# Performance work log

Measured on AMD Instinct MI355X. Metric: run time of the kernel, lower is better.

## Reference

```python
import jax, jax.numpy as jnp
import numpy as np

T = 512          # tokens
H = 2048         # hidden_size
E = 256          # n_routed_experts (8 groups x 32)
G = 8            # tucker groups
EPG = 32         # experts per group
K = 6            # top_k
I = 1408         # moe_intermediate_size
R1 = 128         # tucker input rank
R2 = 128         # tucker output rank


def setup_inputs() -> dict:
    key = jax.random.key(0)
    ks = jax.random.split(key, 12)
    s = 0.02
    return {
        "hidden_states": jax.random.normal(ks[0], (T, H), jnp.float32),
        "w_router": jax.random.normal(ks[1], (H, E), jnp.float32) * s,
        # gate_proj Tucker factors: H -> I
        "U_in_gate": jax.random.normal(ks[2], (G, H, R1), jnp.float32) * s,
        "core_gate": jax.random.normal(ks[3], (E, R1, R2), jnp.float32) * s,
        "U_out_gate": jax.random.normal(ks[4], (G, I, R2), jnp.float32) * s,
        # up_proj Tucker factors: H -> I
        "U_in_up": jax.random.normal(ks[5], (G, H, R1), jnp.float32) * s,
        "core_up": jax.random.normal(ks[6], (E, R1, R2), jnp.float32) * s,
        "U_out_up": jax.random.normal(ks[7], (G, I, R2), jnp.float32) * s,
        # down_proj Tucker factors: I -> H
        "U_in_down": jax.random.normal(ks[8], (G, I, R1), jnp.float32) * s,
        "core_down": jax.random.normal(ks[9], (E, R1, R2), jnp.float32) * s,
        "U_out_down": jax.random.normal(ks[10], (G, H, R2), jnp.float32) * s,
    }


def _tucker_apply(x, g, e, U_in, core, U_out):
    """Per-expert Tucker linear: y_t = ((x_t @ U_in[g_t]) @ core[e_t]) @ U_out[g_t].T
    x: [Td, din]; g: [Td] group ids; e: [Td] full expert ids.
    U_in: [G, din, r1]; core: [E, r1, r2]; U_out: [G, dout, r2]."""
    h1 = jnp.einsum('td,gdr->tgr', x, U_in)                       # [Td, G, r1]
    h1 = jnp.take_along_axis(h1, g[:, None, None], axis=1)[:, 0]  # [Td, r1]
    h2 = jnp.einsum('tr,trs->ts', h1, core[e])                    # [Td, r2]
    y = jnp.einsum('ts,gds->tgd', h2, U_out)                      # [Td, G, dout]
    return jnp.take_along_axis(y, g[:, None, None], axis=1)[:, 0]


def reference(hidden_states, w_router, U_in_gate, core_gate, U_out_gate,
              U_in_up, core_up, U_out_up, U_in_down, core_down, U_out_down):
    n_tok, hid = hidden_states.shape
    router_logits = hidden_states @ w_router                          # [T, E]
    probs = jax.nn.softmax(router_logits.astype(jnp.float32), axis=-1)
    routing_weights, selected = jax.lax.top_k(probs, K)               # [T, K]
    routing_weights = routing_weights / routing_weights.sum(-1, keepdims=True)
    routing_weights = routing_weights.astype(hidden_states.dtype)

    xd = jnp.repeat(hidden_states, K, axis=0)                         # [T*K, H]
    e = selected.reshape(-1)                                          # [T*K]
    g = e // EPG                                                      # group ids

    gate_out = _tucker_apply(xd, g, e, U_in_gate, core_gate, U_out_gate)
    up_out = _tucker_apply(xd, g, e, U_in_up, core_up, U_out_up)
    inter = jax.nn.silu(gate_out) * up_out                            # [T*K, I]
    down_out = _tucker_apply(inter, g, e, U_in_down, core_down, U_out_down)

    combined = (down_out.reshape(n_tok, K, hid) * routing_weights[..., None]).sum(axis=1)
    return combined
```

## Files before the change

### kernel.cpp

```cpp
#include <hip/hip_runtime.h>
#include <cmath>
#include <cstdint>

#define TNUM 512
#define HID 2048
#define NEXP 256
#define NGRP 8
#define KTOP 6
#define IDIM 1408
#define RNK 128
#define NPAIR (TNUM*KTOP)
#define NRCAP 3328
#define MAXTILES (NRCAP/32)

typedef _Float16 f16;
typedef f16  f16x8 __attribute__((ext_vector_type(8)));
typedef f16  f16x4 __attribute__((ext_vector_type(4)));
typedef float f32x4 __attribute__((ext_vector_type(4)));
#define MFMA16(a,b,c) __builtin_amdgcn_mfma_f32_16x16x32_f16((a),(b),(c),0,0,0)

static __device__ __forceinline__ float4 ld4(const float* p){ return *reinterpret_cast<const float4*>(p); }
static __device__ __forceinline__ void st4(float* p, float4 v){ *reinterpret_cast<float4*>(p) = v; }
static __device__ __forceinline__ f16x8 ldh8(const f16* p){ return *reinterpret_cast<const f16x8*>(p); }

constexpr size_t A256(size_t x){ return (x + 255) & ~(size_t)255; }
constexpr size_t OFF_SEL    = 0;
constexpr size_t OFF_WT     = A256(OFF_SEL    + (size_t)NPAIR*4);
constexpr size_t OFF_CNT    = A256(OFF_WT     + (size_t)NPAIR*4);
constexpr size_t OFF_ESTART = A256(OFF_CNT    + (size_t)NEXP*4);
constexpr size_t OFF_TG     = A256(OFF_ESTART + (size_t)NEXP*4);
constexpr size_t OFF_HDR    = A256(OFF_TG     + (size_t)MAXTILES*4);
constexpr size_t OFF_ROWT   = A256(OFF_HDR    + 16);
constexpr size_t OFF_POS    = A256(OFF_ROWT   + (size_t)NRCAP*4);
constexpr size_t OFF_BIG    = A256(OFF_POS    + (size_t)NPAIR*4);

constexpr size_t SZ_XH    = (size_t)TNUM*HID*2;
constexpr size_t SZ_UTI   = (size_t)NGRP*RNK*HID*2;
constexpr size_t SZ_H1ALL = (size_t)2*TNUM*NGRP*RNK*2;
constexpr size_t SZ_UO    = (size_t)NGRP*IDIM*RNK*2;
constexpr size_t SZ_UOD   = (size_t)NGRP*HID*RNK*2;
constexpr size_t SZ_WR    = (size_t)NEXP*HID*2;
constexpr size_t SZ_H2    = (size_t)NRCAP*RNK*2;
constexpr size_t SZ_DOWNO = (size_t)NRCAP*HID*2;

constexpr size_t OFF_XH    = OFF_BIG;
constexpr size_t OFF_XL    = OFF_XH   + SZ_XH;
constexpr size_t OFF_UTIG  = OFF_XL   + SZ_XH;
constexpr size_t OFF_UTIU  = OFF_UTIG + SZ_UTI;
constexpr size_t OFF_H1    = OFF_UTIU + SZ_UTI;
constexpr size_t REG_END   = OFF_H1   + SZ_H1ALL;
constexpr size_t OFF_DOWNO = OFF_XH;
constexpr size_t OFF_LPART = OFF_H1;
constexpr size_t OFF_UOG   = REG_END;
constexpr size_t OFF_UOU   = OFF_UOG  + SZ_UO;
constexpr size_t OFF_UTID  = OFF_UOU  + SZ_UO;
constexpr size_t OFF_UOD   = OFF_UTID + SZ_UO;
constexpr size_t OFF_WRH   = OFF_UOD  + SZ_UOD;
constexpr size_t OFF_WRL   = OFF_WRH  + SZ_WR;
constexpr size_t OFF_H2G   = OFF_WRL  + SZ_WR;
constexpr size_t OFF_H2U   = OFF_H2G  + SZ_H2;
constexpr size_t OFF_D1P   = OFF_H2U  + SZ_H2;
constexpr size_t OFF_D2    = OFF_D1P  + 4*SZ_H2;
constexpr size_t WS_NEED   = OFF_D2   + SZ_H2;
static_assert(OFF_DOWNO + SZ_DOWNO <= OFF_UOG, "downo overlay must end before persistent tail");

__global__ __launch_bounds__(256) void k_cvt(
    const float* __restrict__ x,   const float* __restrict__ Uog,
    const float* __restrict__ Uou, const float* __restrict__ Uod,
    const float* __restrict__ wr,
    const float* __restrict__ Uig, const float* __restrict__ Uiu, const float* __restrict__ Uid,
    f16* __restrict__ xh, f16* __restrict__ xl,
    f16* __restrict__ uog, f16* __restrict__ uou, f16* __restrict__ uod,
    f16* __restrict__ wh, f16* __restrict__ wl,
    f16* __restrict__ ig, f16* __restrict__ iu, f16* __restrict__ idn,
    int* __restrict__ cnt){
  __shared__ float tile[32][33];
  const int b = blockIdx.x, tid = threadIdx.x;
  if(b < 1024){
    const size_t i = (size_t)b*256 + tid;
    float4 v = ld4(x + i*4);
    f16x4 H, L;
    H[0]=(f16)v.x; L[0]=(f16)(v.x-(float)H[0]);
    H[1]=(f16)v.y; L[1]=(f16)(v.y-(float)H[1]);
    H[2]=(f16)v.z; L[2]=(f16)(v.z-(float)H[2]);
    H[3]=(f16)v.w; L[3]=(f16)(v.w-(float)H[3]);
    *reinterpret_cast<f16x4*>(xh + i*4) = H;
    *reinterpret_cast<f16x4*>(xl + i*4) = L;
    return;
  }
  if(b < 5888){
    const float* in; f16* hi; size_t i;
    if(b < 2432){        in = Uog; hi = uog; i = (size_t)(b-1024)*256 + tid; }
    else if(b < 3840){   in = Uou; hi = uou; i = (size_t)(b-2432)*256 + tid; }
    else {               in = Uod; hi = uod; i = (size_t)(b-3840)*256 + tid; }
    float4 v = ld4(in + i*4);
    f16x4 H;
    H[0]=(f16)(v.x*16.f); H[1]=(f16)(v.y*16.f); H[2]=(f16)(v.z*16.f); H[3]=(f16)(v.w*16.f);
    *reinterpret_cast<f16x4*>(hi + i*4) = H;
    return;
  }
  if(b < 6400){
    const int wb = b - 5888;
    if(wb == 0) cnt[tid] = 0;
    const int c0 = (wb & 7)*32, r0 = (wb >> 3)*32;
    { const int r = tid>>3, c4 = (tid&7)*4;
      float4 v = ld4(wr + (size_t)(r0+r)*NEXP + c0 + c4);
      tile[r][c4]=v.x; tile[r][c4+1]=v.y; tile[r][c4+2]=v.z; tile[r][c4+3]=v.w; }
    __syncthreads();
    { const int c = tid>>3, r4 = (tid&7)*4;
      f16x4 H, L;
      #pragma unroll
      for(int k = 0; k < 4; k++){
        float v = tile[r4+k][c]*16.f;
        H[k] = (f16)v; L[k] = (f16)(v - (float)H[k]);
      }
      const size_t o = (size_t)(c0+c)*HID + r0 + r4;
      *reinterpret_cast<f16x4*>(wh + o) = H;
      *reinterpret_cast<f16x4*>(wl + o) = L; }
    return;
  }
  const int b2 = b - 6400;
  const int cx = b2 & 3, ry = (b2>>2) & 63, z = b2 >> 8;
  const int tensor = z >> 3, g = z & 7;
  const float* in; f16* o; int R;
  if(tensor == 0){ in = Uig; o = ig; R = HID; }
  else if(tensor == 1){ in = Uiu; o = iu; R = HID; }
  else { in = Uid; o = idn; R = IDIM; }
  const int r0 = ry*32, c0 = cx*32;
  if(r0 >= R) return;
  in += (size_t)g*R*RNK; o += (size_t)g*RNK*R;
  { const int r = tid>>3, c4 = (tid&7)*4;
    float4 v = ld4(in + (size_t)(r0+r)*RNK + c0 + c4);
    tile[r][c4]=v.x; tile[r][c4+1]=v.y; tile[r][c4+2]=v.z; tile[r][c4+3]=v.w; }
  __syncthreads();
  { const int c = tid>>3, r4 = (tid&7)*4;
    f16x4 H;
    #pragma unroll
    for(int k = 0; k < 4; k++) H[k] = (f16)(tile[r4+k][c]*16.f);
    *reinterpret_cast<f16x4*>(o + (size_t)(c0+c)*R + r0 + r4) = H; }
}

__global__ __launch_bounds__(256) void k_router_mfma(
    const f16* __restrict__ xh, const f16* __restrict__ xl,
    const f16* __restrict__ wh, const f16* __restrict__ wl,
    float* __restrict__ lpart){
  __shared__ float red[4][32][64];
  const int m = blockIdx.x, ecol = blockIdx.y, kz = blockIdx.z;
  const int tid = threadIdx.x;
  const int wid = tid>>6, lane = tid&63, q = lane>>4, id = lane&15;
  const int r0 = m*32, e0 = ecol*64;
  const int kb = kz*512 + wid*128;
  f32x4 acc[2][4];
  #pragma unroll
  for(int f = 0; f < 2; f++)
    #pragma unroll
    for(int c = 0; c < 4; c++) acc[f][c] = (f32x4){0.f,0.f,0.f,0.f};
  #pragma unroll
  for(int kk = 0; kk < 128; kk += 32){
    const size_t a0 = (size_t)(r0+id)*HID    + kb + kk + q*8;
    const size_t a1 = (size_t)(r0+16+id)*HID + kb + kk + q*8;
    f16x8 ah0 = ldh8(xh + a0), al0 = ldh8(xl + a0);
    f16x8 ah1 = ldh8(xh + a1), al1 = ldh8(xl + a1);
    #pragma unroll
    for(int c = 0; c < 4; c++){
      const size_t bo = (size_t)(e0 + c*16 + id)*HID + kb + kk + q*8;
      f16x8 bh = ldh8(wh + bo);
      f16x8 bl = ldh8(wl + bo);
      acc[0][c] = MFMA16(ah0, bh, acc[0][c]);
      acc[0][c] = MFMA16(ah0, bl, acc[0][c]);
      acc[0][c] = MFMA16(al0, bh, acc[0][c]);
      acc[1][c] = MFMA16(ah1, bh, acc[1][c]);
      acc[1][c] = MFMA16(ah1, bl, acc[1][c]);
      acc[1][c] = MFMA16(al1, bh, acc[1][c]);
    }
  }
  #pragma unroll
  for(int f = 0; f < 2; f++)
    #pragma unroll
    for(int c = 0; c < 4; c++)
      #pragma unroll
      for(int r = 0; r < 4; r++)
        red[wid][f*16 + q*4 + r][c*16 + id] = acc[f][c][r];
  __syncthreads();
  const int row = tid>>3, c8 = (tid&7)*8;
  float o[8];
  #pragma unroll
  for(int j = 0; j < 8; j++)
    o[j] = (red[0][row][c8+j] + red[1][row][c8+j] + red[2][row][c8+j] + red[3][row][c8+j])*0.0625f;
  float* dst = &lpart[((size_t)kz*TNUM + r0 + row)*NEXP + e0 + c8];
  st4(dst,     make_float4(o[0],o[1],o[2],o[3]));
  st4(dst + 4, make_float4(o[4],o[5],o[6],o[7]));
}

__global__ __launch_bounds__(256) void k_topk(const float* __restrict__ lpart,
                                              int* __restrict__ sel,
                                              float* __restrict__ wt,
                                              int* __restrict__ cnt){
  __shared__ float wv[4];
  __shared__ int   wi[4];
  __shared__ float swin[KTOP];
  __shared__ int   iwin[KTOP];
  const int t = blockIdx.x, tid = threadIdx.x;
  const int lane = tid & 63, wid = tid >> 6;
  const size_t base = (size_t)t*NEXP + tid;
  float v = lpart[base] + lpart[base + (size_t)TNUM*NEXP]
          + lpart[base + (size_t)2*TNUM*NEXP] + lpart[base + (size_t)3*TNUM*NEXP];
  for(int k = 0; k < KTOP; k++){
    float cv = v; int ci = tid;
    #pragma unroll
    for(int off = 1; off < 64; off <<= 1){
      float ov = __shfl_xor(cv, off);
      int   oi = __shfl_xor(ci, off);
      if(ov > cv || (ov == cv && oi < ci)){ cv = ov; ci = oi; }
    }
    if(lane == 0){ wv[wid] = cv; wi[wid] = ci; }
    __syncthreads();
    if(tid == 0){
      float bv = wv[0]; int bi = wi[0];
      #pragma unroll
      for(int w2 = 1; w2 < 4; w2++)
        if(wv[w2] > bv || (wv[w2] == bv && wi[w2] < bi)){ bv = wv[w2]; bi = wi[w2]; }
      swin[k] = bv; iwin[k] = bi;
    }
    __syncthreads();
    if(tid == iwin[k]) v = -INFINITY;
  }
  if(tid == 0){
    float mx = swin[0], s = 0.f, ww[KTOP];
    #pragma unroll
    for(int k = 0; k < KTOP; k++){ ww[k] = expf(swin[k]-mx); s += ww[k]; }
    float inv = 1.f/s;
    #pragma unroll
    for(int k = 0; k < KTOP; k++){
      sel[t*KTOP+k] = iwin[k];
      wt[t*KTOP+k]  = ww[k]*inv;
      atomicAdd(&cnt[iwin[k]], 1);
    }
  }
}

__global__ __launch_bounds__(256) void k_meta_scatter(
    const int* __restrict__ cnt, const int* __restrict__ sel,
    int* __restrict__ estart, int* __restrict__ tile_group, int* __restrict__ hdr,
    int* __restrict__ row_t, int* __restrict__ pos_of_pair){
  __shared__ int scnt[256];
  __shared__ int gsum[8];
  __shared__ int g0[9];
  __shared__ int curs[256];
  const int tid = threadIdx.x;
  scnt[tid] = cnt[tid];
  if(tid < 8) gsum[tid] = 0;
  __syncthreads();
  atomicAdd(&gsum[tid>>5], scnt[tid]);
  __syncthreads();
  if(tid == 0){
    int run = 0;
    for(int g = 0; g < 8; g++){ g0[g] = run; run += (gsum[g]+31) & ~31; }
    g0[8] = run; hdr[0] = run>>5; hdr[1] = run;
  }
  __syncthreads();
  int g = tid >> 5, s = g0[g];
  for(int i = (g<<5); i < tid; i++) s += scnt[i];
  estart[tid] = s; curs[tid] = s;
  const int nt = g0[8] >> 5;
  for(int t2 = tid; t2 < MAXTILES; t2 += 256){
    int gg = -1;
    if(t2 < nt){
      for(int g2 = 0; g2 < 8; g2++) if(t2*32 >= g0[g2] && t2*32 < g0[g2+1]) gg = g2;
    }
    tile_group[t2] = gg;
  }
  __syncthreads();
  for(int p = tid; p < NPAIR; p += 256){
    const int e = sel[p];
    const int pos = atomicAdd(&curs[e], 1);
    row_t[pos] = p / KTOP;
    pos_of_pair[p] = pos;
  }
}

__global__ __launch_bounds__(256) void k_mm_stage1(
    const f16* __restrict__ xh,
    const f16* __restrict__ Bg_, const f16* __restrict__ Bu_,
    f16* __restrict__ H1){
  __shared__ float red[4][32][64];
  const int nt = blockIdx.x, m = blockIdx.y;
  const int pu = nt>>4, g = (nt>>1)&7, ch = nt&1;
  const f16* B = (pu ? Bu_ : Bg_) + (size_t)g*RNK*HID + (size_t)ch*64*HID;
  const int tid = threadIdx.x;
  const int wid = tid>>6, lane = tid&63, q = lane>>4, id = lane&15;
  const int kb = wid*512;
  const int r0 = m*32;
  f32x4 acc[2][4];
  #pragma unroll
  for(int f = 0; f < 2; f++)
    #pragma unroll
    for(int c = 0; c < 4; c++) acc[f][c] = (f32x4){0.f,0.f,0.f,0.f};
  #pragma unroll 4
  for(int kk = 0; kk < 512; kk += 32){
    f16x8 a0 = ldh8(xh + (size_t)(r0+id)*HID    + kb + kk + q*8);
    f16x8 a1 = ldh8(xh + (size_t)(r0+16+id)*HID + kb + kk + q*8);
    #pragma unroll
    for(int c = 0; c < 4; c++){
      f16x8 b = ldh8(B + (size_t)(c*16+id)*HID + kb + kk + q*8);
      acc[0][c] = MFMA16(a0, b, acc[0][c]);
      acc[1][c] = MFMA16(a1, b, acc[1][c]);
    }
  }
  #pragma unroll
  for(int f = 0; f < 2; f++)
    #pragma unroll
    for(int c = 0; c < 4; c++)
      #pragma unroll
      for(int r = 0; r < 4; r++)
        red[wid][f*16 + q*4 + r][c*16 + id] = acc[f][c][r];
  __syncthreads();
  f16* out = H1 + (size_t)pu*TNUM*(NGRP*RNK);
  const int row = tid>>3, c8 = (tid&7)*8;
  f16x8 o8;
  #pragma unroll
  for(int j = 0; j < 8; j++)
    o8[j] = (f16)(red[0][row][c8+j] + red[1][row][c8+j] + red[2][row][c8+j] + red[3][row][c8+j]);
  *reinterpret_cast<f16x8*>(&out[(size_t)(r0+row)*(NGRP*RNK) + g*RNK + ch*64 + c8]) = o8;
}

__global__ __launch_bounds__(256) void k_core2(
    const float* __restrict__ Cg, const float* __restrict__ Cu,
    const f16* __restrict__ H1,
    const int* __restrict__ estart, const int* __restrict__ cnt,
    const int* __restrict__ row_t,
    f16* __restrict__ h2g, f16* __restrict__ h2u){
  __shared__ f16 Cs[RNK][RNK+8];
  __shared__ float tile[32][33];
  const int e = blockIdx.x, up = blockIdx.y;
  const int n = cnt[e];
  if(n == 0) return;
  const float* Cf = (up ? Cu : Cg) + (size_t)e*RNK*RNK;
  const int tid = threadIdx.x;
  #pragma unroll 2
  for(int st = 0; st < 16; st++){
    const int R0 = (st>>2)*32, C0 = (st&3)*32;
    { const int r = tid>>3, c4 = (tid&7)*4;
      float4 v = ld4(Cf + (size_t)(R0+r)*RNK + C0 + c4);
      tile[r][c4]=v.x; tile[r][c4+1]=v.y; tile[r][c4+2]=v.z; tile[r][c4+3]=v.w; }
    __syncthreads();
    { const int c = tid>>3, r4 = (tid&7)*4;
      f16x4 H;
      #pragma unroll
      for(int k2 = 0; k2 < 4; k2++) H[k2] = (f16)(tile[r4+k2][c]*16.f);
      *reinterpret_cast<f16x4*>(&Cs[C0+c][R0+r4]) = H; }
    __syncthreads();
  }
  const int j0 = estart[e], g = e >> 5;
  const f16* A = H1 + (size_t)up*TNUM*(NGRP*RNK);
  f16* o = up ? h2u : h2g;
  const int wid = tid>>6, lane = tid&63, q = lane>>4, id = lane&15;
  for(int rt = 0; rt*16 < n; rt++){
    const int jrow = j0 + rt*16 + id;
    const int jj = jrow < j0+n ? jrow : j0;
    const f16* arow = A + (size_t)row_t[jj]*(NGRP*RNK) + g*RNK;
    f32x4 acc0 = (f32x4){0.f,0.f,0.f,0.f};
    f32x4 acc1 = (f32x4){0.f,0.f,0.f,0.f};
    #pragma unroll
    for(int kk = 0; kk < RNK; kk += 32){
      f16x8 a = ldh8(arow + kk + q*8);
      f16x8 b0 = *reinterpret_cast<const f16x8*>(&Cs[wid*32 + id][kk + q*8]);
      f16x8 b1 = *reinterpret_cast<const f16x8*>(&Cs[wid*32 + 16 + id][kk + q*8]);
      acc0 = MFMA16(a, b0, acc0);
      acc1 = MFMA16(a, b1, acc1);
    }
    #pragma unroll
    for(int r = 0; r < 4; r++){
      const int j = j0 + rt*16 + q*4 + r;
      if(j < j0+n){
        o[(size_t)j*RNK + wid*32 + id]      = (f16)acc0[r];
        o[(size_t)j*RNK + wid*32 + 16 + id] = (f16)acc1[r];
      }
    }
  }
}

__global__ __launch_bounds__(256) void k_gateup_downin(
    const f16* __restrict__ Ag, const f16* __restrict__ Au,
    const f16* __restrict__ Bg, const f16* __restrict__ Bu,
    const f16* __restrict__ Bd,
    const int* __restrict__ tg,
    f16* __restrict__ d1p){
  __shared__ f16 inter_s[32][360];
  const int g = tg[blockIdx.x];
  if(g < 0) return;
  const int j0 = blockIdx.x*32, qz = blockIdx.y;
  const int cbase = qz*352;
  const int tid = threadIdx.x, wid = tid>>6, lane = tid&63, q = lane>>4, id = lane&15;
  const size_t bbase = (size_t)g*IDIM*RNK;
  f16x8 aG[2][4], aU[2][4];
  #pragma unroll
  for(int f = 0; f < 2; f++)
    #pragma unroll
    for(int k4 = 0; k4 < 4; k4++){
      const size_t off = (size_t)(j0 + f*16 + id)*RNK + k4*32 + q*8;
      aG[f][k4] = ldh8(Ag + off);
      aU[f][k4] = ldh8(Au + off);
    }
  for(int t = wid; t < 22; t += 4){
    const int c0 = cbase + t*16;
    f32x4 accg0 = (f32x4){0.f,0.f,0.f,0.f}, accg1 = (f32x4){0.f,0.f,0.f,0.f};
    f32x4 accu0 = (f32x4){0.f,0.f,0.f,0.f}, accu1 = (f32x4){0.f,0.f,0.f,0.f};
    #pragma unroll
    for(int k4 = 0; k4 < 4; k4++){
      const size_t bo = bbase + (size_t)(c0 + id)*RNK + k4*32 + q*8;
      f16x8 bg = ldh8(Bg + bo);
      f16x8 bu = ldh8(Bu + bo);
      accg0 = MFMA16(aG[0][k4], bg, accg0);
      accg1 = MFMA16(aG[1][k4], bg, accg1);
      accu0 = MFMA16(aU[0][k4], bu, accu0);
      accu1 = MFMA16(aU[1][k4], bu, accu1);
    }
    #pragma unroll
    for(int r = 0; r < 4; r++){
      float vg0 = accg0[r]*(1.f/4096.f), vu0 = accu0[r]*(1.f/4096.f);
      float vg1 = accg1[r]*(1.f/4096.f), vu1 = accu1[r]*(1.f/4096.f);
      inter_s[q*4+r][t*16+id]    = (f16)(vg0/(1.f+expf(-vg0))*vu0*256.f);
      inter_s[16+q*4+r][t*16+id] = (f16)(vg1/(1.f+expf(-vg1))*vu1*256.f);
    }
  }
  __syncthreads();
  const int col0 = wid*32;
  f32x4 acc[2][2];
  #pragma unroll
  for(int f = 0; f < 2; f++)
    #pragma unroll
    for(int c = 0; c < 2; c++) acc[f][c] = (f32x4){0.f,0.f,0.f,0.f};
  const f16* Bdg = Bd + (size_t)g*RNK*IDIM;
  #pragma unroll 2
  for(int kk = 0; kk < 352; kk += 32){
    f16x8 a0 = *reinterpret_cast<const f16x8*>(&inter_s[id][kk + q*8]);
    f16x8 a1 = *reinterpret_cast<const f16x8*>(&inter_s[16+id][kk + q*8]);
    #pragma unroll
    for(int c = 0; c < 2; c++){
      f16x8 b = ldh8(Bdg + (size_t)(col0 + c*16 + id)*IDIM + cbase + kk + q*8);
      acc[0][c] = MFMA16(a0, b, acc[0][c]);
      acc[1][c] = MFMA16(a1, b, acc[1][c]);
    }
  }
  f16* out = d1p + (size_t)qz*NRCAP*RNK;
  #pragma unroll
  for(int f = 0; f < 2; f++)
    #pragma unroll
    for(int c = 0; c < 2; c++)
      #pragma unroll
      for(int r = 0; r < 4; r++)
        out[(size_t)(j0 + f*16 + q*4 + r)*RNK + col0 + c*16 + id] = (f16)acc[f][c][r];
}

__global__ __launch_bounds__(256) void k_core_down(
    const float* __restrict__ Cd,
    const f16* __restrict__ d1p,
    const int* __restrict__ estart, const int* __restrict__ cnt,
    f16* __restrict__ d2){
  __shared__ f16 Cs[RNK][RNK+8];
  __shared__ float tile[32][33];
  const int e = blockIdx.x;
  const int n = cnt[e];
  if(n == 0) return;
  const float* Cf = Cd + (size_t)e*RNK*RNK;
  const int tid = threadIdx.x;
  #pragma unroll 2
  for(int st = 0; st < 16; st++){
    const int R0 = (st>>2)*32, C0 = (st&3)*32;
    { const int r = tid>>3, c4 = (tid&7)*4;
      float4 v = ld4(Cf + (size_t)(R0+r)*RNK + C0 + c4);
      tile[r][c4]=v.x; tile[r][c4+1]=v.y; tile[r][c4+2]=v.z; tile[r][c4+3]=v.w; }
    __syncthreads();
    { const int c = tid>>3, r4 = (tid&7)*4;
      f16x4 H;
      #pragma unroll
      for(int k2 = 0; k2 < 4; k2++) H[k2] = (f16)(tile[r4+k2][c]*16.f);
      *reinterpret_cast<f16x4*>(&Cs[C0+c][R0+r4]) = H; }
    __syncthreads();
  }
  const int j0 = estart[e];
  const size_t PL = (size_t)NRCAP*RNK;
  const int wid = tid>>6, lane = tid&63, q = lane>>4, id = lane&15;
  for(int rt = 0; rt*16 < n; rt++){
    const int jrow = j0 + rt*16 + id;
    const int jj = jrow < j0+n ? jrow : j0;
    const size_t arow = (size_t)jj*RNK;
    f32x4 acc0 = (f32x4){0.f,0.f,0.f,0.f};
    f32x4 acc1 = (f32x4){0.f,0.f,0.f,0.f};
    #pragma unroll
    for(int kk = 0; kk < RNK; kk += 32){
      const size_t off = arow + kk + q*8;
      f16x8 a = ldh8(d1p + off);
      a += ldh8(d1p + off + PL);
      a += ldh8(d1p + off + 2*PL);
      a += ldh8(d1p + off + 3*PL);
      f16x8 b0 = *reinterpret_cast<const f16x8*>(&Cs[wid*32 + id][kk + q*8]);
      f16x8 b1 = *reinterpret_cast<const f16x8*>(&Cs[wid*32 + 16 + id][kk + q*8]);
      acc0 = MFMA16(a, b0, acc0);
      acc1 = MFMA16(a, b1, acc1);
    }
    #pragma unroll
    for(int r = 0; r < 4; r++){
      const int j = j0 + rt*16 + q*4 + r;
      if(j < j0+n){
        d2[(size_t)j*RNK + wid*32 + id]      = (f16)acc0[r];
        d2[(size_t)j*RNK + wid*32 + 16 + id] = (f16)acc1[r];
      }
    }
  }
}

__global__ __launch_bounds__(128) void k_mm_down_out(
    const f16* __restrict__ A_, const f16* __restrict__ B_,
    const int* __restrict__ tg,
    f16* __restrict__ downo){
  const int g = tg[blockIdx.x];
  if(g < 0) return;
  const int j0 = blockIdx.x*32;
  const f16* B = B_ + (size_t)g*HID*RNK;
  const int tid = threadIdx.x;
  const int wid = tid>>6, lane = tid&63, q = lane>>4, id = lane&15;
  const int c0 = blockIdx.y*128 + wid*64;
  f32x4 acc[2][4];
  #pragma unroll
  for(int f = 0; f < 2; f++)
    #pragma unroll
    for(int c = 0; c < 4; c++) acc[f][c] = (f32x4){0.f,0.f,0.f,0.f};
  #pragma unroll 2
  for(int kk = 0; kk < RNK; kk += 32){
    f16x8 a0 = ldh8(A_ + (size_t)(j0+id)*RNK    + kk + q*8);
    f16x8 a1 = ldh8(A_ + (size_t)(j0+16+id)*RNK + kk + q*8);
    #pragma unroll
    for(int c = 0; c < 4; c++){
      f16x8 b = ldh8(B + (size_t)(c0 + c*16 + id)*RNK + kk + q*8);
      acc[0][c] = MFMA16(a0, b, acc[0][c]);
      acc[1][c] = MFMA16(a1, b, acc[1][c]);
    }
  }
  #pragma unroll
  for(int f = 0; f < 2; f++)
    #pragma unroll
    for(int c = 0; c < 4; c++)
      #pragma unroll
      for(int r = 0; r < 4; r++)
        downo[(size_t)(j0 + f*16 + q*4 + r)*HID + c0 + c*16 + id] = (f16)(acc[f][c][r]*(1.f/1024.f));
}

__global__ __launch_bounds__(256) void k_combine(const f16* __restrict__ downo,
                                                 const int* __restrict__ pos_of_pair,
                                                 const float* __restrict__ wt,
                                                 float* __restrict__ out){
  const int idx = blockIdx.x*256 + threadIdx.x;
  const int t  = idx >> 9;
  const int h4 = (idx & 511) << 2;
  float4 acc = make_float4(0.f,0.f,0.f,0.f);
  #pragma unroll
  for(int k = 0; k < KTOP; k++){
    const int p = t*KTOP + k;
    const float w = wt[p]*(1.f/1024.f);
    const int pos = pos_of_pair[p];
    f16x4 v = *reinterpret_cast<const f16x4*>(&downo[(size_t)pos*HID + h4]);
    acc.x += w*(float)v[0]; acc.y += w*(float)v[1];
    acc.z += w*(float)v[2]; acc.w += w*(float)v[3];
  }
  st4(&out[(size_t)t*HID + h4], acc);
}

extern "C" void kernel_launch(void* const* d_in, const int* in_sizes, int n_in,
                              void* d_out, int out_size, void* d_ws, size_t ws_size,
                              hipStream_t stream){
  const float* x   = (const float*)d_in[0];
  const float* wr  = (const float*)d_in[1];
  const float* Uig = (const float*)d_in[2];
  const float* cg  = (const float*)d_in[3];
  const float* Uog = (const float*)d_in[4];
  const float* Uiu = (const float*)d_in[5];
  const float* cu  = (const float*)d_in[6];
  const float* Uou = (const float*)d_in[7];
  const float* Uid = (const float*)d_in[8];
  const float* cd  = (const float*)d_in[9];
  const float* Uod = (const float*)d_in[10];
  float* out = (float*)d_out;
  char* ws = (char*)d_ws;
  if(ws_size < WS_NEED) return;

  int*   sel    = (int*)  (ws + OFF_SEL);
  float* wt     = (float*)(ws + OFF_WT);
  int*   cnt    = (int*)  (ws + OFF_CNT);
  int*   estart = (int*)  (ws + OFF_ESTART);
  int*   tg     = (int*)  (ws + OFF_TG);
  int*   hdr    = (int*)  (ws + OFF_HDR);
  int*   row_t  = (int*)  (ws + OFF_ROWT);
  int*   pos    = (int*)  (ws + OFF_POS);
  float* lpart  = (float*)(ws + OFF_LPART);
  f16* xh    = (f16*)(ws + OFF_XH);
  f16* xl    = (f16*)(ws + OFF_XL);
  f16* utig  = (f16*)(ws + OFF_UTIG);
  f16* utiu  = (f16*)(ws + OFF_UTIU);
  f16* H1    = (f16*)(ws + OFF_H1);
  f16* uog   = (f16*)(ws + OFF_UOG);
  f16* uou   = (f16*)(ws + OFF_UOU);
  f16* utid  = (f16*)(ws + OFF_UTID);
  f16* uod   = (f16*)(ws + OFF_UOD);
  f16* wrh   = (f16*)(ws + OFF_WRH);
  f16* wrl   = (f16*)(ws + OFF_WRL);
  f16* h2g   = (f16*)(ws + OFF_H2G);
  f16* h2u   = (f16*)(ws + OFF_H2U);
  f16* d1p   = (f16*)(ws + OFF_D1P);
  f16* d2    = (f16*)(ws + OFF_D2);
  f16* downo = (f16*)(ws + OFF_DOWNO);

  k_cvt      <<<12544,             256, 0, stream>>>(x, Uog, Uou, Uod, wr, Uig, Uiu, Uid,
                                                     xh, xl, uog, uou, uod, wrh, wrl,
                                                     utig, utiu, utid, cnt);

  k_router_mfma<<<dim3(16,4,4),    256, 0, stream>>>(xh, xl, wrh, wrl, lpart);
  k_topk     <<<TNUM,              256, 0, stream>>>(lpart, sel, wt, cnt);
  k_meta_scatter<<<1,              256, 0, stream>>>(cnt, sel, estart, tg, hdr, row_t, pos);

  k_mm_stage1<<<dim3(32,16),       256, 0, stream>>>(xh, utig, utiu, H1);
  k_core2    <<<dim3(NEXP,2),      256, 0, stream>>>(cg, cu, H1, estart, cnt, row_t, h2g, h2u);
  k_gateup_downin<<<dim3(MAXTILES,4),256,0, stream>>>(h2g, h2u, uog, uou, utid, tg, d1p);
  k_core_down<<<NEXP,              256, 0, stream>>>(cd, d1p, estart, cnt, d2);
  k_mm_down_out<<<dim3(MAXTILES,16),128,0, stream>>>(d2, uod, tg, downo);
  k_combine  <<<1024,              256, 0, stream>>>(downo, pos, wt, out);
}
```

Before: 136.7 us.

## Fuse top-k and routing metadata via last-block counter; narrow stage1 tiles

The separate single-block metadata scatter kernel is folded into the top-k kernel. Each block increments a global done counter after a threadfence, and the last block to finish builds the expert offsets, tile groups and row mappings. This removes one kernel launch and its gap. Separately, stage-1 projection tiles shrink from 64 to 32 output columns, doubling the grid to 1024 blocks for better occupancy, at the cost of reloading the activation rows twice as often.

Result: slower. 150.1 us (+9.9%).

```diff
diff --git a/kernel.cpp b/kernel.cpp
--- a/kernel.cpp
+++ b/kernel.cpp
@@ -30,7 +30,8 @@
 constexpr size_t OFF_ESTART = A256(OFF_CNT    + (size_t)NEXP*4);
 constexpr size_t OFF_TG     = A256(OFF_ESTART + (size_t)NEXP*4);
 constexpr size_t OFF_HDR    = A256(OFF_TG     + (size_t)MAXTILES*4);
-constexpr size_t OFF_ROWT   = A256(OFF_HDR    + 16);
+constexpr size_t OFF_DONE   = A256(OFF_HDR    + 16);
+constexpr size_t OFF_ROWT   = A256(OFF_DONE   + 16);
 constexpr size_t OFF_POS    = A256(OFF_ROWT   + (size_t)NRCAP*4);
 constexpr size_t OFF_BIG    = A256(OFF_POS    + (size_t)NPAIR*4);
 
@@ -73,7 +74,7 @@
     f16* __restrict__ uog, f16* __restrict__ uou, f16* __restrict__ uod,
     f16* __restrict__ wh, f16* __restrict__ wl,
     f16* __restrict__ ig, f16* __restrict__ iu, f16* __restrict__ idn,
-    int* __restrict__ cnt){
+    int* __restrict__ cnt, int* __restrict__ done){
   __shared__ float tile[32][33];
   const int b = blockIdx.x, tid = threadIdx.x;
   if(b < 1024){
@@ -101,7 +102,7 @@
   }
   if(b < 6400){
     const int wb = b - 5888;
-    if(wb == 0) cnt[tid] = 0;
+    if(wb == 0){ cnt[tid] = 0; if(tid == 0) done[0] = 0; }
     const int c0 = (wb & 7)*32, r0 = (wb >> 3)*32;
     { const int r = tid>>3, c4 = (tid&7)*4;
       float4 v = ld4(wr + (size_t)(r0+r)*NEXP + c0 + c4);
@@ -192,14 +193,21 @@
   st4(dst + 4, make_float4(o[4],o[5],o[6],o[7]));
 }
 
-__global__ __launch_bounds__(256) void k_topk(const float* __restrict__ lpart,
-                                              int* __restrict__ sel,
-                                              float* __restrict__ wt,
-                                              int* __restrict__ cnt){
+__global__ __launch_bounds__(256) void k_topk_meta(
+    const float* __restrict__ lpart,
+    int* __restrict__ sel, float* __restrict__ wt, int* __restrict__ cnt,
+    int* __restrict__ done,
+    int* __restrict__ estart, int* __restrict__ tile_group, int* __restrict__ hdr,
+    int* __restrict__ row_t, int* __restrict__ pos_of_pair){
   __shared__ float wv[4];
   __shared__ int   wi[4];
   __shared__ float swin[KTOP];
   __shared__ int   iwin[KTOP];
+  __shared__ int   lastflag;
+  __shared__ int scnt[256];
+  __shared__ int gsum[8];
+  __shared__ int g0[9];
+  __shared__ int curs[256];
   const int t = blockIdx.x, tid = threadIdx.x;
   const int lane = tid & 63, wid = tid >> 6;
   const size_t base = (size_t)t*NEXP + tid;
@@ -236,18 +244,13 @@
       wt[t*KTOP+k]  = ww[k]*inv;
       atomicAdd(&cnt[iwin[k]], 1);
     }
-  }
-}
-
-__global__ __launch_bounds__(256) void k_meta_scatter(
-    const int* __restrict__ cnt, const int* __restrict__ sel,
-    int* __restrict__ estart, int* __restrict__ tile_group, int* __restrict__ hdr,
-    int* __restrict__ row_t, int* __restrict__ pos_of_pair){
-  __shared__ int scnt[256];
-  __shared__ int gsum[8];
-  __shared__ int g0[9];
-  __shared__ int curs[256];
-  const int tid = threadIdx.x;
+    __threadfence();
+    const int old = atomicAdd(done, 1);
+    lastflag = (old == TNUM-1) ? 1 : 0;
+  }
+  __syncthreads();
+  if(!lastflag) return;
+  __threadfence();
   scnt[tid] = cnt[tid];
   if(tid < 8) gsum[tid] = 0;
   __syncthreads();
@@ -283,25 +286,25 @@
     const f16* __restrict__ xh,
     const f16* __restrict__ Bg_, const f16* __restrict__ Bu_,
     f16* __restrict__ H1){
-  __shared__ float red[4][32][64];
+  __shared__ float red[4][32][32];
   const int nt = blockIdx.x, m = blockIdx.y;
-  const int pu = nt>>4, g = (nt>>1)&7, ch = nt&1;
-  const f16* B = (pu ? Bu_ : Bg_) + (size_t)g*RNK*HID + (size_t)ch*64*HID;
+  const int pu = nt>>5, g = (nt>>2)&7, ch = nt&3;
+  const f16* B = (pu ? Bu_ : Bg_) + (size_t)g*RNK*HID + (size_t)ch*32*HID;
   const int tid = threadIdx.x;
   const int wid = tid>>6, lane = tid&63, q = lane>>4, id = lane&15;
   const int kb = wid*512;
   const int r0 = m*32;
-  f32x4 acc[2][4];
-  #pragma unroll
-  for(int f = 0; f < 2; f++)
-    #pragma unroll
-    for(int c = 0; c < 4; c++) acc[f][c] = (f32x4){0.f,0.f,0.f,0.f};
+  f32x4 acc[2][2];
+  #pragma unroll
+  for(int f = 0; f < 2; f++)
+    #pragma unroll
+    for(int c = 0; c < 2; c++) acc[f][c] = (f32x4){0.f,0.f,0.f,0.f};
   #pragma unroll 4
   for(int kk = 0; kk < 512; kk += 32){
     f16x8 a0 = ldh8(xh + (size_t)(r0+id)*HID    + kb + kk + q*8);
     f16x8 a1 = ldh8(xh + (size_t)(r0+16+id)*HID + kb + kk + q*8);
     #pragma unroll
-    for(int c = 0; c < 4; c++){
+    for(int c = 0; c < 2; c++){
       f16x8 b = ldh8(B + (size_t)(c*16+id)*HID + kb + kk + q*8);
       acc[0][c] = MFMA16(a0, b, acc[0][c]);
       acc[1][c] = MFMA16(a1, b, acc[1][c]);
@@ -310,18 +313,18 @@
   #pragma unroll
   for(int f = 0; f < 2; f++)
     #pragma unroll
-    for(int c = 0; c < 4; c++)
+    for(int c = 0; c < 2; c++)
       #pragma unroll
       for(int r = 0; r < 4; r++)
         red[wid][f*16 + q*4 + r][c*16 + id] = acc[f][c][r];
   __syncthreads();
   f16* out = H1 + (size_t)pu*TNUM*(NGRP*RNK);
-  const int row = tid>>3, c8 = (tid&7)*8;
-  f16x8 o8;
-  #pragma unroll
-  for(int j = 0; j < 8; j++)
-    o8[j] = (f16)(red[0][row][c8+j] + red[1][row][c8+j] + red[2][row][c8+j] + red[3][row][c8+j]);
-  *reinterpret_cast<f16x8*>(&out[(size_t)(r0+row)*(NGRP*RNK) + g*RNK + ch*64 + c8]) = o8;
+  const int row = tid>>3, c4 = (tid&7)*4;
+  f16x4 o4;
+  #pragma unroll
+  for(int j = 0; j < 4; j++)
+    o4[j] = (f16)(red[0][row][c4+j] + red[1][row][c4+j] + red[2][row][c4+j] + red[3][row][c4+j]);
+  *reinterpret_cast<f16x4*>(&out[(size_t)(r0+row)*(NGRP*RNK) + g*RNK + ch*32 + c4]) = o4;
 }
 
 __global__ __launch_bounds__(256) void k_core2(
@@ -591,6 +594,7 @@
   int*   estart = (int*)  (ws + OFF_ESTART);
   int*   tg     = (int*)  (ws + OFF_TG);
   int*   hdr    = (int*)  (ws + OFF_HDR);
+  int*   done   = (int*)  (ws + OFF_DONE);
   int*   row_t  = (int*)  (ws + OFF_ROWT);
   int*   pos    = (int*)  (ws + OFF_POS);
   float* lpart  = (float*)(ws + OFF_LPART);
@@ -613,13 +617,13 @@
 
   k_cvt      <<<12544,             256, 0, stream>>>(x, Uog, Uou, Uod, wr, Uig, Uiu, Uid,
                                                      xh, xl, uog, uou, uod, wrh, wrl,
-                                                     utig, utiu, utid, cnt);
+                                                     utig, utiu, utid, cnt, done);
 
   k_router_mfma<<<dim3(16,4,4),    256, 0, stream>>>(xh, xl, wrh, wrl, lpart);
-  k_topk     <<<TNUM,              256, 0, stream>>>(lpart, sel, wt, cnt);
-  k_meta_scatter<<<1,              256, 0, stream>>>(cnt, sel, estart, tg, hdr, row_t, pos);
-
-  k_mm_stage1<<<dim3(32,16),       256, 0, stream>>>(xh, utig, utiu, H1);
+  k_topk_meta<<<TNUM,              256, 0, stream>>>(lpart, sel, wt, cnt, done,
+                                                     estart, tg, hdr, row_t, pos);
+
+  k_mm_stage1<<<dim3(64,16),       256, 0, stream>>>(xh, utig, utiu, H1);
   k_core2    <<<dim3(NEXP,2),      256, 0, stream>>>(cg, cu, H1, estart, cnt, row_t, h2g, h2u);
   k_gateup_downin<<<dim3(MAXTILES,4),256,0, stream>>>(h2g, h2u, uog, uou, utid, tg, d1p);
   k_core_down<<<NEXP,              256, 0, stream>>>(cd, d1p, estart, cnt, d2);
```
